# Kernel optimization log

Hardware: AMD Instinct MI355X
Metric: run time of the kernel (lower is better)

## Reference

```python
import jax, jax.numpy as jnp
import numpy as np

B, S, I, H = 2, 400, 80, 128
F = 2 * H            # bidirectional feature dim
N = S + 1            # zero row prepended -> pairwise grid size
MAX_SEG = 50
NCLS = 50


def prelu(x, a):
    return jnp.where(x >= 0, x, a * x)


def lstm_dir(x, Wi, Wh, b, reverse=False):
    # x: (B, S, I); torch gate order: i, f, g, o
    if reverse:
        x = x[:, ::-1]
    Hd = Wh.shape[1]

    def step(carry, xt):
        h, c = carry
        gates = xt @ Wi.T + h @ Wh.T + b
        i_, f_, g_, o_ = jnp.split(gates, 4, axis=-1)
        c = jax.nn.sigmoid(f_) * c + jax.nn.sigmoid(i_) * jnp.tanh(g_)
        h = jax.nn.sigmoid(o_) * jnp.tanh(c)
        return (h, c), h

    h0 = jnp.zeros((x.shape[0], Hd), x.dtype)
    _, hs = jax.lax.scan(step, (h0, h0), jnp.swapaxes(x, 0, 1))
    hs = jnp.swapaxes(hs, 0, 1)
    if reverse:
        hs = hs[:, ::-1]
    return hs


def setup_inputs() -> dict:
    key = jax.random.key(0)
    ks = jax.random.split(key, 16)

    def rn(k, shape, s=0.05):
        return jax.random.normal(k, shape, jnp.float32) * s

    inp = {
        "x": jax.random.normal(ks[0], (B, S, I), jnp.float32),
        "lengths": jnp.full((B,), S, jnp.int32),
        "Wi_f": rn(ks[1], (4 * H, I)), "Wh_f": rn(ks[2], (4 * H, H)), "b_f": jnp.zeros((4 * H,), jnp.float32),
        "Wi_b": rn(ks[3], (4 * H, I)), "Wh_b": rn(ks[4], (4 * H, H)), "b_b": jnp.zeros((4 * H,), jnp.float32),
        "a1": jnp.full((1,), 0.25, jnp.float32),
        "W1": rn(ks[5], (100, 3 * F)), "b1": jnp.zeros((100,), jnp.float32),
        "a2": jnp.full((1,), 0.25, jnp.float32),
        "W2": rn(ks[6], (1, 100)), "b2": jnp.zeros((1,), jnp.float32),
        "ac1": jnp.full((1,), 0.25, jnp.float32),
        "Wc1": rn(ks[7], (2 * NCLS, F)), "bc1": jnp.zeros((2 * NCLS,), jnp.float32),
        "ac2": jnp.full((1,), 0.25, jnp.float32),
        "Wc2": rn(ks[8], (NCLS, 2 * NCLS)), "bc2": jnp.zeros((NCLS,), jnp.float32),
        "ab1": jnp.full((1,), 0.25, jnp.float32),
        "Wb1": rn(ks[9], (2 * NCLS, F)), "bb1": jnp.zeros((2 * NCLS,), jnp.float32),
        "ab2": jnp.full((1,), 0.25, jnp.float32),
        "Wb2": rn(ks[10], (2, 2 * NCLS)), "bb2": jnp.zeros((2,), jnp.float32),
    }
    return inp


def compute_scores(x, Wi_f, Wh_f, b_f, Wi_b, Wh_b, b_b, a1, W1, b1, a2, W2, b2):
    rnn_out = jnp.concatenate(
        [lstm_dir(x, Wi_f, Wh_f, b_f, False), lstm_dir(x, Wi_b, Wh_b, b_b, True)], axis=-1
    )  # (B, S, F)
    xp = jnp.concatenate([jnp.zeros((x.shape[0], 1, F), x.dtype), rnn_out], axis=1)  # (B, N, F)
    cum = jnp.cumsum(xp, axis=1)
    # phi[b,i,j] = concat(cum[j]-cum[i], xp[i], xp[j]); PReLU is elementwise with a
    # single shared parameter, and the first Linear is additive across the concat
    # blocks, so we decompose W1 instead of materializing the (B,N,N,3F) tensor.
    W1c, W1d, W1e = W1[:, :F], W1[:, F:2 * F], W1[:, 2 * F:]
    pc = prelu(cum[:, None, :, :] - cum[:, :, None, :], a1)  # (B, N, N, F)
    pxd = prelu(xp, a1) @ W1d.T                              # (B, N, 100)
    pxe = prelu(xp, a1) @ W1e.T                              # (B, N, 100)
    h = jnp.einsum('bijf,kf->bijk', pc, W1c) + pxd[:, :, None, :] + pxe[:, None, :, :] + b1
    scores = (prelu(h, a2) @ W2.T + b2)[..., 0]              # (B, N, N)
    return rnn_out, scores


def segment_search(scores):
    # DP: best[i] = max_{max(0,i-MAX_SEG) <= k < i} best[k] + scores[:, k, i]
    Bn, Nn = scores.shape[0], scores.shape[1]
    ks = jnp.arange(Nn)

    def dp_step(best, i):
        col = jnp.take(scores, i, axis=2)                    # (B, N)
        mask = (ks >= i - MAX_SEG) & (ks < i)
        cand = jnp.where(mask[None, :], best + col, -jnp.inf)
        m = cand.max(axis=1)
        k = cand.argmax(axis=1)
        best = best.at[:, i].set(m)
        return best, k

    best0 = jnp.zeros((Bn, Nn), scores.dtype)
    best, prev_tail = jax.lax.scan(dp_step, best0, jnp.arange(1, Nn))
    prev = jnp.concatenate([jnp.zeros((Bn, 1), jnp.int32),
                            prev_tail.T.astype(jnp.int32)], axis=1)  # (B, N)
    return best, prev


def reference(x, lengths, Wi_f, Wh_f, b_f, Wi_b, Wh_b, b_b, a1, W1, b1, a2, W2, b2,
              ac1, Wc1, bc1, ac2, Wc2, bc2, ab1, Wb1, bb1, ab2, Wb2, bb2):
    rnn_out, scores = compute_scores(x, Wi_f, Wh_f, b_f, Wi_b, Wh_b, b_b,
                                     a1, W1, b1, a2, W2, b2)
    cls_out = prelu(prelu(rnn_out, ac1) @ Wc1.T + bc1, ac2) @ Wc2.T + bc2
    bin_out = prelu(prelu(rnn_out, ab1) @ Wb1.T + bb1, ab2) @ Wb2.T + bb2
    best, prev = segment_search(scores)
    # pred score for the best segmentation ending at `lengths[b]` equals best[b, L]
    pred_scores = best[jnp.arange(scores.shape[0]), lengths]
    return scores, cls_out, bin_out, pred_scores, prev
```

## Files before the change

### kernel.cpp

```cpp
#include <hip/hip_runtime.h>
#include <hip/hip_fp16.h>
#include <math.h>

#define BB 2
#define SS 400
#define II 80
#define HH 128
#define FF 256
#define NN 401
#define G4 512
#define MAXSEG 50
#define NCLS 50
#define KH 100
#define KP 112
#define FRAGF 14336

#define SCORES_OFF 0
#define CLS_OFF    (BB*NN*NN)
#define BIN_OFF    (CLS_OFF + BB*SS*NCLS)
#define PRED_OFF   (BIN_OFF + BB*SS*2)
#define PREV_OFF   (PRED_OFF + BB)

#define WS_GX      0
#define WS_RNN     (WS_GX + 4*SS*G4)
#define WS_CUM     (WS_RNN + BB*SS*FF)
#define WS_PXD     (WS_CUM + BB*NN*FF)
#define WS_PXE     (WS_PXD + BB*NN*KP)
#define WS_PART    (WS_PXE + BB*NN*KP)
#define WS_W2P     (WS_PART + BB*16*FF)
#define WS_B1P     (WS_W2P + KP)
#define WS_WHP     (WS_B1P + KP)
#define WS_WFRAGC  (WS_WHP + 65536)
#define WS_WFRAGD  (WS_WFRAGC + FRAGF)
#define WS_WFRAGE  (WS_WFRAGD + FRAGF)
#define WS_WFRAGHC (WS_WFRAGE + FRAGF)
#define WS_WFRAGHB (WS_WFRAGHC + FRAGF)
#define WS_BC1P    (WS_WFRAGHB + FRAGF)
#define WS_BB1P    (WS_BC1P + KP)

typedef __attribute__((ext_vector_type(8))) short short8;
typedef __attribute__((ext_vector_type(4))) float f32x4;
typedef _Float16 f16x2 __attribute__((ext_vector_type(2)));
typedef _Float16 f16x8 __attribute__((ext_vector_type(8)));

__device__ __forceinline__ float prelu_f(float x, float a) {
    return x >= 0.f ? x : a * x;
}
__device__ __forceinline__ unsigned short f2bf(float x) {
    union { float f; unsigned u; } v; v.f = x;
    unsigned r = v.u + 0x7fffu + ((v.u >> 16) & 1u);
    return (unsigned short)(r >> 16);
}
__device__ __forceinline__ float fast_sigmoid(float x) {
    return 1.f / (1.f + __expf(-x));
}
__device__ __forceinline__ float fast_tanh(float x) {
    return 1.f - 2.f / (1.f + __expf(2.f * x));
}
__device__ __forceinline__ void barrier_lds() {
    asm volatile("s_waitcnt lgkmcnt(0)\ns_barrier" ::: "memory");
}
__device__ __forceinline__ void rec_barrier() {
    __builtin_amdgcn_sched_barrier(0);
    asm volatile("s_waitcnt lgkmcnt(0)");
    __builtin_amdgcn_s_barrier();
    __builtin_amdgcn_sched_barrier(0);
}
__device__ __forceinline__ int fragidx(int k, int f) {
    int kt = k >> 4, l15 = k & 15;
    int ks = f >> 5, quad = (f >> 3) & 3, e = f & 7;
    return ((((kt * 8 + ks) * 4 + quad) * 16) + l15) * 8 + e;
}

#define WPACKS (5 * KP)
#define PREPBLKS (WPACKS + G4)
__global__ void k_lstm_pre(const float* __restrict__ x,
                           const float* __restrict__ Wi_f, const float* __restrict__ b_f,
                           const float* __restrict__ Wi_b, const float* __restrict__ b_b,
                           float* __restrict__ gx,
                           const float* __restrict__ W1, const float* __restrict__ W2,
                           const float* __restrict__ b1,
                           const float* __restrict__ Wh_f, const float* __restrict__ Wh_b,
                           const float* __restrict__ Wc1, const float* __restrict__ Wb1,
                           const float* __restrict__ bc1, const float* __restrict__ bb1,
                           short* __restrict__ wfC, short* __restrict__ wfD,
                           short* __restrict__ wfE, short* __restrict__ wfHC,
                           short* __restrict__ wfHB,
                           float* __restrict__ w2p, float* __restrict__ b1p,
                           float* __restrict__ bc1p, float* __restrict__ bb1p,
                           __half* __restrict__ whp) {
    int blk0 = blockIdx.x;
    int tid = threadIdx.x;
    if (blk0 < WPACKS) {
        int which = blk0 / KP;
        int k = blk0 % KP;
        float w = 0.f;
        short* dst = wfC;
        if (which == 0)      { if (k < KH) w = W1[k * (3 * FF) + tid];          dst = wfC; }
        else if (which == 1) { if (k < KH) w = W1[k * (3 * FF) + FF + tid];     dst = wfD; }
        else if (which == 2) { if (k < KH) w = W1[k * (3 * FF) + 2 * FF + tid]; dst = wfE; }
        else if (which == 3) { if (k < KH) w = Wc1[k * FF + tid];               dst = wfHC; }
        else                 { if (k < KH) w = Wb1[k * FF + tid];               dst = wfHB; }
        dst[fragidx(k, tid)] = (short)f2bf(w);
        if (tid == 0) {
            if (which == 0) {
                w2p[k] = (k < KH) ? W2[k] : 0.f;
                b1p[k] = (k < KH) ? b1[k] : 0.f;
            } else if (which == 3) {
                bc1p[k] = (k < KH) ? bc1[k] : 0.f;
            } else if (which == 4) {
                bb1p[k] = (k < KH) ? bb1[k] : 0.f;
            }
        }
        return;
    }
    if (blk0 < PREPBLKS) {
        int gq = blk0 - WPACKS;
        int gate = gq >> 7;
        int unit = gq & 127;
        int wv = unit >> 4, col = unit & 15;
        int dir = tid >> 7, k = tid & 127;
        int kt = k >> 5, lanehi = (k >> 3) & 3, e = k & 7;
        int lane = lanehi * 16 + col;
        const float* Wh = dir ? Wh_b : Wh_f;
        whp[(size_t)(((((dir * 4 + gate) * 8 + wv) * 4 + kt) * 64) + lane) * 8 + e] =
            (__half)Wh[gq * HH + k];
        return;
    }
    int blk = blk0 - PREPBLKS;
    int t = blk % SS;
    int db = blk / SS;
    int b = db & 1, dir = db >> 1;
    const float* Wi = dir ? Wi_b : Wi_f;
    const float* bias = dir ? b_b : b_f;
    int xt = dir ? (SS - 1 - t) : t;

    __shared__ __align__(16) float xr[II];
    if (tid < II) xr[tid] = x[(b * SS + xt) * II + tid];
    __syncthreads();

    for (int g = tid; g < G4; g += 256) {
        const float* w = Wi + g * II;
        float acc = bias[g];
#pragma unroll
        for (int i = 0; i < II; i += 4) {
            float4 w4 = *(const float4*)(w + i);
            acc += w4.x * xr[i] + w4.y * xr[i + 1] + w4.z * xr[i + 2] + w4.w * xr[i + 3];
        }
        gx[((size_t)(db * SS + t) * HH + (g & 127)) * 4 + (g >> 7)] = acc;
    }
}

__global__ __launch_bounds__(256, 1)
void k_lstm_rec(const _Float16* __restrict__ whf, const float* __restrict__ gxr,
                float* __restrict__ rnn_out) {
    int db = blockIdx.x;
    int b = db & 1, dir = db >> 1;
    int tid = threadIdx.x;
    int wv = tid >> 6;
    int lane = tid & 63;

    f16x8 bfA[4][4], bfB[4][4];
    {
        const f16x8* wp = (const f16x8*)whf;
#pragma unroll
        for (int g = 0; g < 4; ++g)
#pragma unroll
            for (int kt = 0; kt < 4; ++kt) {
                bfA[g][kt] = wp[((((dir * 4 + g) * 8 + (2 * wv)) * 4 + kt) * 64) + lane];
                bfB[g][kt] = wp[((((dir * 4 + g) * 8 + (2 * wv + 1)) * 4 + kt) * 64) + lane];
            }
    }

    __shared__ __align__(16) __half hsf[2][128];
    (&hsf[0][0])[tid] = (__half)0.f;
    __syncthreads();

    bool act = (lane < 32);
    bool grpB = (lane >= 16);
    int unit = (wv << 5) + (lane & 31);
    float c_state = 0.f;

    const float4* gp4 = (const float4*)gxr + (size_t)(db * SS) * HH + unit;
    float4 g0 = make_float4(0,0,0,0), g1 = g0, g2 = g0, g3 = g0;
    if (act) {
        g0 = gp4[0 * HH];
        g1 = gp4[1 * HH];
        g2 = gp4[2 * HH];
        g3 = gp4[3 * HH];
    }
    const float4* gq = gp4 + (size_t)4 * HH;

    float* outp = rnn_out + ((size_t)b * SS + (dir ? (SS - 1) : 0)) * FF
                + dir * HH + unit;
    const int ostep = dir ? -FF : FF;

    const f32x4 z4 = (f32x4){0.f, 0.f, 0.f, 0.f};
    int pb = 0;
    int hib = (lane >> 4) * 8;
    bool aload = (lane & 3) == 0;

    f16x8 a0v = (f16x8)(_Float16)0.f, a1v = a0v, a2v = a0v, a3v = a0v;

#define REC_STEP(G, PF) do {                                                   \
        if (aload) {                                                           \
            a0v = *(const f16x8*)(&hsf[pb][ 0 + hib]);                         \
            a1v = *(const f16x8*)(&hsf[pb][32 + hib]);                         \
            a2v = *(const f16x8*)(&hsf[pb][64 + hib]);                         \
            a3v = *(const f16x8*)(&hsf[pb][96 + hib]);                         \
        }                                                                      \
        f32x4 aA0 = __builtin_amdgcn_mfma_f32_16x16x32_f16(a0v, bfA[0][0], z4, 0, 0, 0); \
        f32x4 aA1 = __builtin_amdgcn_mfma_f32_16x16x32_f16(a0v, bfA[1][0], z4, 0, 0, 0); \
        f32x4 aA2 = __builtin_amdgcn_mfma_f32_16x16x32_f16(a0v, bfA[2][0], z4, 0, 0, 0); \
        f32x4 aA3 = __builtin_amdgcn_mfma_f32_16x16x32_f16(a0v, bfA[3][0], z4, 0, 0, 0); \
        f32x4 aB0 = __builtin_amdgcn_mfma_f32_16x16x32_f16(a0v, bfB[0][0], z4, 0, 0, 0); \
        f32x4 aB1 = __builtin_amdgcn_mfma_f32_16x16x32_f16(a0v, bfB[1][0], z4, 0, 0, 0); \
        f32x4 aB2 = __builtin_amdgcn_mfma_f32_16x16x32_f16(a0v, bfB[2][0], z4, 0, 0, 0); \
        f32x4 aB3 = __builtin_amdgcn_mfma_f32_16x16x32_f16(a0v, bfB[3][0], z4, 0, 0, 0); \
        aA0 = __builtin_amdgcn_mfma_f32_16x16x32_f16(a1v, bfA[0][1], aA0, 0, 0, 0); \
        aA1 = __builtin_amdgcn_mfma_f32_16x16x32_f16(a1v, bfA[1][1], aA1, 0, 0, 0); \
        aA2 = __builtin_amdgcn_mfma_f32_16x16x32_f16(a1v, bfA[2][1], aA2, 0, 0, 0); \
        aA3 = __builtin_amdgcn_mfma_f32_16x16x32_f16(a1v, bfA[3][1], aA3, 0, 0, 0); \
        aB0 = __builtin_amdgcn_mfma_f32_16x16x32_f16(a1v, bfB[0][1], aB0, 0, 0, 0); \
        aB1 = __builtin_amdgcn_mfma_f32_16x16x32_f16(a1v, bfB[1][1], aB1, 0, 0, 0); \
        aB2 = __builtin_amdgcn_mfma_f32_16x16x32_f16(a1v, bfB[2][1], aB2, 0, 0, 0); \
        aB3 = __builtin_amdgcn_mfma_f32_16x16x32_f16(a1v, bfB[3][1], aB3, 0, 0, 0); \
        aA0 = __builtin_amdgcn_mfma_f32_16x16x32_f16(a2v, bfA[0][2], aA0, 0, 0, 0); \
        aA1 = __builtin_amdgcn_mfma_f32_16x16x32_f16(a2v, bfA[1][2], aA1, 0, 0, 0); \
        aA2 = __builtin_amdgcn_mfma_f32_16x16x32_f16(a2v, bfA[2][2], aA2, 0, 0, 0); \
        aA3 = __builtin_amdgcn_mfma_f32_16x16x32_f16(a2v, bfA[3][2], aA3, 0, 0, 0); \
        aB0 = __builtin_amdgcn_mfma_f32_16x16x32_f16(a2v, bfB[0][2], aB0, 0, 0, 0); \
        aB1 = __builtin_amdgcn_mfma_f32_16x16x32_f16(a2v, bfB[1][2], aB1, 0, 0, 0); \
        aB2 = __builtin_amdgcn_mfma_f32_16x16x32_f16(a2v, bfB[2][2], aB2, 0, 0, 0); \
        aB3 = __builtin_amdgcn_mfma_f32_16x16x32_f16(a2v, bfB[3][2], aB3, 0, 0, 0); \
        aA0 = __builtin_amdgcn_mfma_f32_16x16x32_f16(a3v, bfA[0][3], aA0, 0, 0, 0); \
        aA1 = __builtin_amdgcn_mfma_f32_16x16x32_f16(a3v, bfA[1][3], aA1, 0, 0, 0); \
        aA2 = __builtin_amdgcn_mfma_f32_16x16x32_f16(a3v, bfA[2][3], aA2, 0, 0, 0); \
        aA3 = __builtin_amdgcn_mfma_f32_16x16x32_f16(a3v, bfA[3][3], aA3, 0, 0, 0); \
        aB0 = __builtin_amdgcn_mfma_f32_16x16x32_f16(a3v, bfB[0][3], aB0, 0, 0, 0); \
        aB1 = __builtin_amdgcn_mfma_f32_16x16x32_f16(a3v, bfB[1][3], aB1, 0, 0, 0); \
        aB2 = __builtin_amdgcn_mfma_f32_16x16x32_f16(a3v, bfB[2][3], aB2, 0, 0, 0); \
        aB3 = __builtin_amdgcn_mfma_f32_16x16x32_f16(a3v, bfB[3][3], aB3, 0, 0, 0); \
        if (act) {                                                             \
            float gi = (grpB ? aB0[0] : aA0[0]) + G.x;                         \
            float gf = (grpB ? aB1[0] : aA1[0]) + G.y;                         \
            float gg = (grpB ? aB2[0] : aA2[0]) + G.z;                         \
            float go = (grpB ? aB3[0] : aA3[0]) + G.w;                         \
            if (PF) { G = *gq; gq += HH; }         \
            c_state = fast_sigmoid(gf) * c_state + fast_sigmoid(gi) * fast_tanh(gg); \
            float h = fast_sigmoid(go) * fast_tanh(c_state);                   \
            hsf[pb ^ 1][unit] = (__half)h;                                     \
            *outp = h;                                                         \
            outp += ostep;                                                     \
        }                                                                      \
        rec_barrier();                                                         \
        pb ^= 1;                                                               \
    } while (0)

    for (int it = 0; it < 99; ++it) {
        REC_STEP(g0, 1);
        REC_STEP(g1, 1);
        REC_STEP(g2, 1);
        REC_STEP(g3, 1);
    }
    REC_STEP(g0, 0);
    REC_STEP(g1, 0);
    REC_STEP(g2, 0);
    REC_STEP(g3, 0);
#undef REC_STEP
}

#define PXBLKS 26
#define HDBLKS 25
#define AP 272
#define UCP 116
__global__ __launch_bounds__(256, 2)
void k_cum_mlp(const float* __restrict__ rnn, float* __restrict__ cum,
               const float* __restrict__ a1p,
               const float* __restrict__ ac1p, const float* __restrict__ ab1p,
               const short* __restrict__ wfD, const short* __restrict__ wfE,
               const short* __restrict__ wfHC, const short* __restrict__ wfHB,
               const float* __restrict__ bc1p, const float* __restrict__ bb1p,
               const float* __restrict__ ac2p, const float* __restrict__ ab2p,
               const float* __restrict__ Wc2, const float* __restrict__ bc2,
               const float* __restrict__ Wb2, const float* __restrict__ bb2,
               float* __restrict__ pxd, float* __restrict__ pxe,
               float* __restrict__ cls_out, float* __restrict__ bin_out) {
    int tid = threadIdx.x;
    if (blockIdx.x < BB) {
        int b = blockIdx.x;
        int f = tid;
        float run = 0.f;
        cum[(size_t)(b * NN) * FF + f] = 0.f;
        const float* rp = rnn + (size_t)b * SS * FF + f;
        float* cp = cum + ((size_t)b * NN + 1) * FF + f;
#pragma unroll 8
        for (int t = 0; t < SS; ++t) {
            run += rp[(size_t)t * FF];
            cp[(size_t)t * FF] = run;
        }
        return;
    }
    int blk = blockIdx.x - BB;
    bool is_px = (blk < PXBLKS);
    int rowbase = is_px ? blk * 32 : (blk - PXBLKS) * 32;
    int nrows_tot = is_px ? BB * NN : BB * SS;

    __shared__ __align__(16) short dth[2][32][AP];
    __shared__ float ucsh[2][32][UCP];

    {
        int row = tid >> 3;
        int fb = (tid & 7) * 32;
        int rg = rowbase + row;
        float src[32];
        if (is_px) {
            float a1 = a1p[0];
            int b = rg / NN, n = rg % NN;
            bool valid = (rg < nrows_tot) && (n > 0);
            const float* sp = valid ? (rnn + (b * SS + n - 1) * FF + fb) : nullptr;
#pragma unroll
            for (int c4 = 0; c4 < 8; ++c4) {
                float4 v = valid ? *(const float4*)(sp + c4 * 4) : make_float4(0,0,0,0);
                src[c4*4] = v.x; src[c4*4+1] = v.y; src[c4*4+2] = v.z; src[c4*4+3] = v.w;
            }
            union { short8 s; unsigned short u[8]; } h8;
#pragma unroll
            for (int c8 = 0; c8 < 4; ++c8) {
#pragma unroll
                for (int e = 0; e < 8; ++e) h8.u[e] = f2bf(prelu_f(src[c8*8+e], a1));
                *(short8*)(&dth[0][row][fb + c8 * 8]) = h8.s;
            }
        } else {
            float ac1 = ac1p[0], ab1 = ab1p[0];
            bool valid = (rg < nrows_tot);
            const float* sp = valid ? (rnn + rg * FF + fb) : nullptr;
#pragma unroll
            for (int c4 = 0; c4 < 8; ++c4) {
                float4 v = valid ? *(const float4*)(sp + c4 * 4) : make_float4(0,0,0,0);
                src[c4*4] = v.x; src[c4*4+1] = v.y; src[c4*4+2] = v.z; src[c4*4+3] = v.w;
            }
            union { short8 s; unsigned short u[8]; } hc, hb;
#pragma unroll
            for (int c8 = 0; c8 < 4; ++c8) {
#pragma unroll
                for (int e = 0; e < 8; ++e) {
                    hc.u[e] = f2bf(prelu_f(src[c8*8+e], ac1));
                    hb.u[e] = f2bf(prelu_f(src[c8*8+e], ab1));
                }
                *(short8*)(&dth[0][row][fb + c8 * 8]) = hc.s;
                *(short8*)(&dth[1][row][fb + c8 * 8]) = hb.s;
            }
        }
    }
    __syncthreads();

    int lane = tid & 63;
    int wv = tid >> 6;
    int quad = lane >> 4;
    int l15 = lane & 15;
    int kt0 = wv * 2, kt1 = wv * 2 + 1;
    bool has1 = (kt1 < 7);

    const short8* wp0 = (const short8*)(is_px ? wfD : wfHC);
    const short8* wp1 = (const short8*)(is_px ? wfE : wfHB);

    f32x4 acc[2][2][2];
#pragma unroll
    for (int p = 0; p < 2; ++p)
#pragma unroll
        for (int mt = 0; mt < 2; ++mt)
#pragma unroll
            for (int kk = 0; kk < 2; ++kk) acc[p][mt][kk] = (f32x4){0.f,0.f,0.f,0.f};

#pragma unroll
    for (int ks = 0; ks < 8; ++ks) {
        short8 b00 = wp0[((kt0 * 8 + ks) * 4 + quad) * 16 + l15];
        short8 b01 = has1 ? wp0[((kt1 * 8 + ks) * 4 + quad) * 16 + l15] : b00;
        short8 b10 = wp1[((kt0 * 8 + ks) * 4 + quad) * 16 + l15];
        short8 b11 = has1 ? wp1[((kt1 * 8 + ks) * 4 + quad) * 16 + l15] : b10;
#pragma unroll
        for (int mt = 0; mt < 2; ++mt) {
            short8 a0 = *(const short8*)(&dth[0][mt * 16 + l15][ks * 32 + quad * 8]);
            short8 a1v = is_px ? a0
                       : *(const short8*)(&dth[1][mt * 16 + l15][ks * 32 + quad * 8]);
            acc[0][mt][0] = __builtin_amdgcn_mfma_f32_16x16x32_bf16(a0, b00, acc[0][mt][0], 0, 0, 0);
            acc[1][mt][0] = __builtin_amdgcn_mfma_f32_16x16x32_bf16(a1v, b10, acc[1][mt][0], 0, 0, 0);
            if (has1) {
                acc[0][mt][1] = __builtin_amdgcn_mfma_f32_16x16x32_bf16(a0, b01, acc[0][mt][1], 0, 0, 0);
                acc[1][mt][1] = __builtin_amdgcn_mfma_f32_16x16x32_bf16(a1v, b11, acc[1][mt][1], 0, 0, 0);
            }
        }
    }

    int kout0 = kt0 * 16 + l15;
    int kout1 = has1 ? (kt1 * 16 + l15) : 0;

    if (is_px) {
#pragma unroll
        for (int mt = 0; mt < 2; ++mt) {
#pragma unroll
            for (int r = 0; r < 4; ++r) {
                int m = mt * 16 + quad * 4 + r;
                int rg = rowbase + m;
                if (rg < nrows_tot) {
                    pxd[rg * KP + kout0] = acc[0][mt][0][r];
                    pxe[rg * KP + kout0] = acc[1][mt][0][r];
                    if (has1) {
                        pxd[rg * KP + kout1] = acc[0][mt][1][r];
                        pxe[rg * KP + kout1] = acc[1][mt][1][r];
                    }
                }
            }
        }
        return;
    }

    float bc0 = bc1p[kout0], bc1v = bc1p[kout1];
    float bb0 = bb1p[kout0], bb1v = bb1p[kout1];
    float ac2 = ac2p[0], ab2 = ab2p[0];
#pragma unroll
    for (int mt = 0; mt < 2; ++mt) {
#pragma unroll
        for (int r = 0; r < 4; ++r) {
            int m = mt * 16 + quad * 4 + r;
            ucsh[0][m][kout0] = prelu_f(acc[0][mt][0][r] + bc0, ac2);
            ucsh[1][m][kout0] = prelu_f(acc[1][mt][0][r] + bb0, ab2);
            if (has1) {
                ucsh[0][m][kout1] = prelu_f(acc[0][mt][1][r] + bc1v, ac2);
                ucsh[1][m][kout1] = prelu_f(acc[1][mt][1][r] + bb1v, ab2);
            }
        }
    }
    __syncthreads();
    {
        int row = tid >> 3;
        int oc = tid & 7;
        int rg = rowbase + row;
        bool valid = (rg < nrows_tot);
        for (int o = oc; o < NCLS; o += 8) {
            float s = bc2[o];
            const float* w = Wc2 + o * KH;
#pragma unroll 4
            for (int k = 0; k < KH; ++k) s += w[k] * ucsh[0][row][k];
            if (valid) cls_out[rg * NCLS + o] = s;
        }
        if (tid < 64) {
            int row2 = tid >> 1, o = tid & 1;
            int rg2 = rowbase + row2;
            float s = bb2[o];
            const float* w = Wb2 + o * KH;
#pragma unroll 4
            for (int k = 0; k < KH; ++k) s += w[k] * ucsh[1][row2][k];
            if (rg2 < nrows_tot) bin_out[rg2 * 2 + o] = s;
        }
    }
}

#define JT 32
#define JTILES 13
#define NP2 201
#define APS 280
#define CIP 264
__global__ __launch_bounds__(256, 3)
void k_scores(const float* __restrict__ cum,
              const short* __restrict__ wfrag,
              const float* __restrict__ pxd, const float* __restrict__ pxe,
              const float* __restrict__ b1p, const float* __restrict__ w2p,
              const float* __restrict__ b2p,
              const float* __restrict__ a1p, const float* __restrict__ a2p,
              float* __restrict__ scores, float* __restrict__ dpcol) {
    int blk = blockIdx.x;
    int jt = blk % JTILES;
    int ipair = (blk / JTILES) % NP2;
    int b = blk / (JTILES * NP2);
    int tid = threadIdx.x;
    float a1 = a1p[0], a2 = a2p[0];
    int jbase = jt * JT;
    int i0 = ipair * 2;
    int i1 = i0 + 1;
    bool has_i1 = (i1 <= SS);
    int i1c = has_i1 ? i1 : i0;

    __shared__ __align__(16) float cish[2][CIP];
    __shared__ __align__(16) short dth[2][JT][APS];
    __shared__ float red[2][4][JT];

    cish[0][tid + (tid >> 5)] = cum[(b * NN + i0) * FF + tid];
    cish[1][tid + (tid >> 5)] = cum[(b * NN + i1c) * FF + tid];
    __syncthreads();

    {
        int row = tid >> 3;
        int fb = (tid & 7) * 32;
        int fbq = fb + (tid & 7);
        int jg = jbase + row;
        int jc = (jg <= SS) ? jg : SS;
        const float* cj = cum + (b * NN + jc) * FF + fb;
        float4 v[8];
#pragma unroll
        for (int c8 = 0; c8 < 4; ++c8) {
            v[2 * c8] = *(const float4*)(cj + c8 * 8);
            v[2 * c8 + 1] = *(const float4*)(cj + c8 * 8 + 4);
        }
#pragma unroll
        for (int ii = 0; ii < 2; ++ii) {
            const float* cio = &cish[ii][0];
#pragma unroll
            for (int c8 = 0; c8 < 4; ++c8) {
                float dv[8] = { v[2*c8].x, v[2*c8].y, v[2*c8].z, v[2*c8].w,
                                v[2*c8+1].x, v[2*c8+1].y, v[2*c8+1].z, v[2*c8+1].w };
                union { short8 s; unsigned short u[8]; } h8;
#pragma unroll
                for (int e = 0; e < 8; ++e) {
                    float d = prelu_f(dv[e] - cio[fbq + c8 * 8 + e], a1);
                    h8.u[e] = f2bf(d);
                }
                *(short8*)(&dth[ii][row][fb + c8 * 8]) = h8.s;
            }
        }
    }
    __syncthreads();

    int lane = tid & 63;
    int wv = tid >> 6;
    int quad = lane >> 4;
    int l15 = lane & 15;
    int kt0 = wv * 2, kt1 = wv * 2 + 1;
    bool has1 = (kt1 < 7);

    const short8* wf = (const short8*)wfrag;
    f32x4 acc[2][2][2];
#pragma unroll
    for (int ii = 0; ii < 2; ++ii)
#pragma unroll
        for (int mt = 0; mt < 2; ++mt)
#pragma unroll
            for (int kk = 0; kk < 2; ++kk) acc[ii][mt][kk] = (f32x4){0.f,0.f,0.f,0.f};

#pragma unroll
    for (int ks = 0; ks < 8; ++ks) {
        short8 b0 = wf[((kt0 * 8 + ks) * 4 + quad) * 16 + l15];
        short8 b1v = has1 ? wf[((kt1 * 8 + ks) * 4 + quad) * 16 + l15] : b0;
#pragma unroll
        for (int ii = 0; ii < 2; ++ii) {
#pragma unroll
            for (int mt = 0; mt < 2; ++mt) {
                short8 a = *(const short8*)(&dth[ii][mt * 16 + l15][ks * 32 + quad * 8]);
                acc[ii][mt][0] = __builtin_amdgcn_mfma_f32_16x16x32_bf16(a, b0, acc[ii][mt][0], 0, 0, 0);
                if (has1)
                    acc[ii][mt][1] = __builtin_amdgcn_mfma_f32_16x16x32_bf16(a, b1v, acc[ii][mt][1], 0, 0, 0);
            }
        }
    }

    int kout0 = kt0 * 16 + l15;
    int kout1 = has1 ? (kt1 * 16 + l15) : 0;
    float bb0 = b1p[kout0], bb1v = b1p[kout1];
    float w20 = w2p[kout0];
    float w21 = has1 ? w2p[kout1] : 0.f;

#pragma unroll
    for (int ii = 0; ii < 2; ++ii) {
        int iv = ii ? i1c : i0;
        float pd0 = pxd[(b * NN + iv) * KP + kout0];
        float pd1 = pxd[(b * NN + iv) * KP + kout1];
#pragma unroll
        for (int mt = 0; mt < 2; ++mt) {
#pragma unroll
            for (int r = 0; r < 4; ++r) {
                int m = mt * 16 + quad * 4 + r;
                int jg = jbase + m;
                int jc = (jg <= SS) ? jg : SS;
                float pe0 = pxe[(b * NN + jc) * KP + kout0];
                float pe1 = pxe[(b * NN + jc) * KP + kout1];
                float h0 = acc[ii][mt][0][r] + pd0 + pe0 + bb0;
                float s = w20 * prelu_f(h0, a2);
                float h1 = acc[ii][mt][1][r] + pd1 + pe1 + bb1v;
                s += w21 * prelu_f(h1, a2);
                s += __shfl_xor(s, 1);
                s += __shfl_xor(s, 2);
                s += __shfl_xor(s, 4);
                s += __shfl_xor(s, 8);
                if (l15 == 0) red[ii][wv][m] = s;
            }
        }
    }
    __syncthreads();
    if (tid < 2 * JT) {
        int ii = tid >> 5;
        int jl = tid & 31;
        int jg = jbase + jl;
        int iv = ii ? i1 : i0;
        if (jg <= SS && (ii == 0 || has_i1)) {
            float tot = red[ii][0][jl] + red[ii][1][jl] + red[ii][2][jl] + red[ii][3][jl] + b2p[0];
            scores[(b * NN + iv) * NN + jg] = tot;
            int d = jg - iv;
            if (d >= 1 && d <= MAXSEG) {
                dpcol[(b * NN + jg) * 64 + (iv & 63)] = tot;
            }
        }
    }
}

__global__ void k_dp(const float* __restrict__ dpcol, const int* __restrict__ lengths,
                     float* __restrict__ predF, float* __restrict__ prevF) {
    int b = blockIdx.x;
    int lane = threadIdx.x;
    int len = lengths[b];
    if (lane == 0) prevF[b * NN] = 0.f;

    float blr = 0.f;
    float predv = 0.f;

#define LO(I) (((I) > MAXSEG) ? ((I) - MAXSEG) : 0)
#define LOADCOL(ii) \
    ( ((ii) <= SS && (((lane - LO(ii)) & 63) < ((ii) - LO(ii)))) \
        ? dpcol[(b * NN + (ii)) * 64 + lane] : 0.f )

    float u0 = LOADCOL(1), u1 = LOADCOL(2), u2 = LOADCOL(3), u3 = LOADCOL(4);
    float u4 = LOADCOL(5), u5 = LOADCOL(6), u6 = LOADCOL(7), u7 = LOADCOL(8);

#define DPP_MAX(CTRL, v) do {                                                 \
        int _t = __builtin_amdgcn_update_dpp(__float_as_int(v),               \
                     __float_as_int(v), (CTRL), 0xF, 0xF, false);             \
        (v) = fmaxf((v), __int_as_float(_t));                                 \
    } while (0)

#define DP_STEP(I, BUF) do {                                                  \
        int lo_ = LO(I);                                                      \
        int cnt_ = (I) - lo_;                                                 \
        int off_ = (lane - lo_) & 63;                                         \
        float v0_ = (off_ < cnt_) ? blr + BUF : -INFINITY;                    \
        float v_ = v0_;                                                       \
        DPP_MAX(0x111, v_);                                   \
        DPP_MAX(0x112, v_);                                   \
        DPP_MAX(0x114, v_);                                   \
        DPP_MAX(0x118, v_);                                   \
        DPP_MAX(0x142, v_);                                 \
        DPP_MAX(0x143, v_);                                 \
        float m_ = __int_as_float(                                            \
            __builtin_amdgcn_readlane(__float_as_int(v_), 63));               \
        unsigned long long mk_ = __ballot(v0_ == m_);                         \
        int rot_ = lo_ & 63;                                                  \
        unsigned long long mr_ = rot_ ? ((mk_ >> rot_) | (mk_ << (64 - rot_))) \
                                      : mk_;                                  \
        int kb_ = lo_ + (__ffsll(mr_) - 1);                                   \
        if (lane == 0) {                                                      \
            prevF[b * NN + (I)] = (float)kb_;                                 \
            if ((I) == len) predv = m_;                                       \
        }                                                                     \
        if (lane == ((I) & 63)) blr = m_;                                     \
    } while (0)

    for (int i = 1; i <= SS; i += 8) {
        DP_STEP(i, u0);     u0 = LOADCOL(i + 8);
        DP_STEP(i + 1, u1); u1 = LOADCOL(i + 9);
        DP_STEP(i + 2, u2); u2 = LOADCOL(i + 10);
        DP_STEP(i + 3, u3); u3 = LOADCOL(i + 11);
        DP_STEP(i + 4, u4); u4 = LOADCOL(i + 12);
        DP_STEP(i + 5, u5); u5 = LOADCOL(i + 13);
        DP_STEP(i + 6, u6); u6 = LOADCOL(i + 14);
        DP_STEP(i + 7, u7); u7 = LOADCOL(i + 15);
    }
#undef DP_STEP
#undef DPP_MAX
#undef LOADCOL
#undef LO
    if (lane == 0) predF[b] = predv;
}

extern "C" void kernel_launch(void* const* d_in, const int* in_sizes, int n_in,
                              void* d_out, int out_size, void* d_ws, size_t ws_size,
                              hipStream_t stream) {
    const float* x    = (const float*)d_in[0];
    const int* lengths= (const int*)d_in[1];
    const float* Wi_f = (const float*)d_in[2];
    const float* Wh_f = (const float*)d_in[3];
    const float* b_f  = (const float*)d_in[4];
    const float* Wi_b = (const float*)d_in[5];
    const float* Wh_b = (const float*)d_in[6];
    const float* b_b  = (const float*)d_in[7];
    const float* a1   = (const float*)d_in[8];
    const float* W1   = (const float*)d_in[9];
    const float* b1   = (const float*)d_in[10];
    const float* a2   = (const float*)d_in[11];
    const float* W2   = (const float*)d_in[12];
    const float* b2   = (const float*)d_in[13];
    const float* ac1  = (const float*)d_in[14];
    const float* Wc1  = (const float*)d_in[15];
    const float* bc1  = (const float*)d_in[16];
    const float* ac2  = (const float*)d_in[17];
    const float* Wc2  = (const float*)d_in[18];
    const float* bc2  = (const float*)d_in[19];
    const float* ab1  = (const float*)d_in[20];
    const float* Wb1  = (const float*)d_in[21];
    const float* bb1  = (const float*)d_in[22];
    const float* ab2  = (const float*)d_in[23];
    const float* Wb2  = (const float*)d_in[24];
    const float* bb2  = (const float*)d_in[25];

    float* out = (float*)d_out;
    float* scores = out + SCORES_OFF;
    float* cls    = out + CLS_OFF;
    float* bin    = out + BIN_OFF;
    float* pred   = out + PRED_OFF;
    float* prev   = out + PREV_OFF;

    float* ws    = (float*)d_ws;
    float* gx    = ws + WS_GX;
    float* dpcol = ws + WS_GX;
    float* rnn   = ws + WS_RNN;
    float* cum   = ws + WS_CUM;
    float* pxd   = ws + WS_PXD;
    float* pxe   = ws + WS_PXE;
    float* w2p   = ws + WS_W2P;
    float* b1p   = ws + WS_B1P;
    __half* whp  = (__half*)(ws + WS_WHP);
    short* wfC   = (short*)(ws + WS_WFRAGC);
    short* wfD   = (short*)(ws + WS_WFRAGD);
    short* wfE   = (short*)(ws + WS_WFRAGE);
    short* wfHC  = (short*)(ws + WS_WFRAGHC);
    short* wfHB  = (short*)(ws + WS_WFRAGHB);
    float* bc1p  = ws + WS_BC1P;
    float* bb1p  = ws + WS_BB1P;

    k_lstm_pre<<<PREPBLKS + 4 * SS, 256, 0, stream>>>(x, Wi_f, b_f, Wi_b, b_b, gx,
                                                      W1, W2, b1, Wh_f, Wh_b,
                                                      Wc1, Wb1, bc1, bb1,
                                                      wfC, wfD, wfE, wfHC, wfHB,
                                                      w2p, b1p, bc1p, bb1p, whp);
    k_lstm_rec<<<4, 256, 0, stream>>>((const _Float16*)whp, gx, rnn);
    k_cum_mlp<<<BB + PXBLKS + HDBLKS, 256, 0, stream>>>(rnn, cum, a1, ac1, ab1,
                                                        wfD, wfE, wfHC, wfHB,
                                                        bc1p, bb1p, ac2, ab2,
                                                        Wc2, bc2, Wb2, bb2,
                                                        pxd, pxe, cls, bin);
    k_scores<<<BB * NP2 * JTILES, 256, 0, stream>>>(cum, wfC, pxd, pxe, b1p, w2p, b2,
                                                    a1, a2, scores, dpcol);
    k_dp<<<BB, 64, 0, stream>>>(dpcol, lengths, pred, prev);
}
```

Measured before the change: 553.9 us.

## Tile input projection over timesteps, move weight packing into rec kernel, pair DP steps

The input-gate projection now processes 8 timesteps per block, so each thread loads its two weight rows once and reuses them across all 8 steps instead of once per timestep. The MLP weight-fragment packing moves out of the pre kernel and into extra blocks of the recurrent LSTM kernel, where they run alongside the 4 recurrence blocks on otherwise idle CUs. The serial segment DP handles two positions per step: it interleaves two DPP max reductions and fixes up the second position's dependency on the first by reading the score for that edge directly. The paired step adds register pressure and a tie-breaking subtlety in the argmax.

```diff
diff --git a/kernel.cpp b/kernel.cpp
--- a/kernel.cpp
+++ b/kernel.cpp
@@ -57,9 +57,6 @@
 __device__ __forceinline__ float fast_tanh(float x) {
     return 1.f - 2.f / (1.f + __expf(2.f * x));
 }
-__device__ __forceinline__ void barrier_lds() {
-    asm volatile("s_waitcnt lgkmcnt(0)\ns_barrier" ::: "memory");
-}
 __device__ __forceinline__ void rec_barrier() {
     __builtin_amdgcn_sched_barrier(0);
     asm volatile("s_waitcnt lgkmcnt(0)");
@@ -72,26 +69,103 @@
     return ((((kt * 8 + ks) * 4 + quad) * 16) + l15) * 8 + e;
 }
 
-#define WPACKS (5 * KP)
-#define PREPBLKS (WPACKS + G4)
+#define GXTC 8
+#define GXBLKS (4 * (SS / GXTC))
+#define PREPBLKS (G4 + GXBLKS)
 __global__ void k_lstm_pre(const float* __restrict__ x,
                            const float* __restrict__ Wi_f, const float* __restrict__ b_f,
                            const float* __restrict__ Wi_b, const float* __restrict__ b_b,
                            float* __restrict__ gx,
-                           const float* __restrict__ W1, const float* __restrict__ W2,
-                           const float* __restrict__ b1,
                            const float* __restrict__ Wh_f, const float* __restrict__ Wh_b,
-                           const float* __restrict__ Wc1, const float* __restrict__ Wb1,
-                           const float* __restrict__ bc1, const float* __restrict__ bb1,
-                           short* __restrict__ wfC, short* __restrict__ wfD,
-                           short* __restrict__ wfE, short* __restrict__ wfHC,
-                           short* __restrict__ wfHB,
-                           float* __restrict__ w2p, float* __restrict__ b1p,
-                           float* __restrict__ bc1p, float* __restrict__ bb1p,
                            __half* __restrict__ whp) {
     int blk0 = blockIdx.x;
     int tid = threadIdx.x;
-    if (blk0 < WPACKS) {
+    if (blk0 < G4) {
+        int gq = blk0;
+        int gate = gq >> 7;
+        int unit = gq & 127;
+        int wv = unit >> 4, col = unit & 15;
+        int dir = tid >> 7, k = tid & 127;
+        int kt = k >> 5, lanehi = (k >> 3) & 3, e = k & 7;
+        int lane = lanehi * 16 + col;
+        const float* Wh = dir ? Wh_b : Wh_f;
+        whp[(size_t)(((((dir * 4 + gate) * 8 + wv) * 4 + kt) * 64) + lane) * 8 + e] =
+            (__half)Wh[gq * HH + k];
+        return;
+    }
+    int gxb = blk0 - G4;
+    int db = gxb / (SS / GXTC);
+    int tc = gxb % (SS / GXTC);
+    int b = db & 1, dir = db >> 1;
+    const float* Wi = dir ? Wi_b : Wi_f;
+    const float* bias = dir ? b_b : b_f;
+    int t0 = tc * GXTC;
+
+    __shared__ __align__(16) float xs[GXTC][II];
+    for (int idx = tid; idx < GXTC * II; idx += 256) {
+        int tt = idx / II, ii = idx - tt * II;
+        int xt = dir ? (SS - 1 - (t0 + tt)) : (t0 + tt);
+        xs[tt][ii] = x[(b * SS + xt) * II + ii];
+    }
+    __syncthreads();
+
+    int g1 = tid + 256;
+    const float* w0p = Wi + tid * II;
+    const float* w1p = Wi + g1 * II;
+    float acc0[GXTC], acc1[GXTC];
+    {
+        float b0v = bias[tid], b1v = bias[g1];
+#pragma unroll
+        for (int t = 0; t < GXTC; ++t) { acc0[t] = b0v; acc1[t] = b1v; }
+    }
+    for (int kc = 0; kc < 5; ++kc) {
+        float4 wa0 = *(const float4*)(w0p + kc * 16 + 0);
+        float4 wa1 = *(const float4*)(w0p + kc * 16 + 4);
+        float4 wa2 = *(const float4*)(w0p + kc * 16 + 8);
+        float4 wa3 = *(const float4*)(w0p + kc * 16 + 12);
+        float4 wb0 = *(const float4*)(w1p + kc * 16 + 0);
+        float4 wb1 = *(const float4*)(w1p + kc * 16 + 4);
+        float4 wb2 = *(const float4*)(w1p + kc * 16 + 8);
+        float4 wb3 = *(const float4*)(w1p + kc * 16 + 12);
+#pragma unroll
+        for (int t = 0; t < GXTC; ++t) {
+            float4 x0 = *(const float4*)(&xs[t][kc * 16 + 0]);
+            float4 x1 = *(const float4*)(&xs[t][kc * 16 + 4]);
+            float4 x2 = *(const float4*)(&xs[t][kc * 16 + 8]);
+            float4 x3 = *(const float4*)(&xs[t][kc * 16 + 12]);
+            acc0[t] += wa0.x * x0.x + wa0.y * x0.y + wa0.z * x0.z + wa0.w * x0.w;
+            acc0[t] += wa1.x * x1.x + wa1.y * x1.y + wa1.z * x1.z + wa1.w * x1.w;
+            acc0[t] += wa2.x * x2.x + wa2.y * x2.y + wa2.z * x2.z + wa2.w * x2.w;
+            acc0[t] += wa3.x * x3.x + wa3.y * x3.y + wa3.z * x3.z + wa3.w * x3.w;
+            acc1[t] += wb0.x * x0.x + wb0.y * x0.y + wb0.z * x0.z + wb0.w * x0.w;
+            acc1[t] += wb1.x * x1.x + wb1.y * x1.y + wb1.z * x1.z + wb1.w * x1.w;
+            acc1[t] += wb2.x * x2.x + wb2.y * x2.y + wb2.z * x2.z + wb2.w * x2.w;
+            acc1[t] += wb3.x * x3.x + wb3.y * x3.y + wb3.z * x3.z + wb3.w * x3.w;
+        }
+    }
+#pragma unroll
+    for (int t = 0; t < GXTC; ++t) {
+        gx[((size_t)(db * SS + t0 + t) * HH + (tid & 127)) * 4 + (tid >> 7)] = acc0[t];
+        gx[((size_t)(db * SS + t0 + t) * HH + (g1 & 127)) * 4 + (g1 >> 7)] = acc1[t];
+    }
+}
+
+#define WPACKS (5 * KP)
+__global__ __launch_bounds__(256, 1)
+void k_lstm_rec(const _Float16* __restrict__ whf, const float* __restrict__ gxr,
+                float* __restrict__ rnn_out,
+                const float* __restrict__ W1, const float* __restrict__ W2,
+                const float* __restrict__ b1,
+                const float* __restrict__ Wc1, const float* __restrict__ Wb1,
+                const float* __restrict__ bc1, const float* __restrict__ bb1,
+                short* __restrict__ wfC, short* __restrict__ wfD,
+                short* __restrict__ wfE, short* __restrict__ wfHC,
+                short* __restrict__ wfHB,
+                float* __restrict__ w2p, float* __restrict__ b1p,
+                float* __restrict__ bc1p, float* __restrict__ bb1p) {
+    int tid = threadIdx.x;
+    if (blockIdx.x >= 4) {
+        int blk0 = blockIdx.x - 4;
         int which = blk0 / KP;
         int k = blk0 % KP;
         float w = 0.f;
@@ -114,49 +188,8 @@
         }
         return;
     }
-    if (blk0 < PREPBLKS) {
-        int gq = blk0 - WPACKS;
-        int gate = gq >> 7;
-        int unit = gq & 127;
-        int wv = unit >> 4, col = unit & 15;
-        int dir = tid >> 7, k = tid & 127;
-        int kt = k >> 5, lanehi = (k >> 3) & 3, e = k & 7;
-        int lane = lanehi * 16 + col;
-        const float* Wh = dir ? Wh_b : Wh_f;
-        whp[(size_t)(((((dir * 4 + gate) * 8 + wv) * 4 + kt) * 64) + lane) * 8 + e] =
-            (__half)Wh[gq * HH + k];
-        return;
-    }
-    int blk = blk0 - PREPBLKS;
-    int t = blk % SS;
-    int db = blk / SS;
-    int b = db & 1, dir = db >> 1;
-    const float* Wi = dir ? Wi_b : Wi_f;
-    const float* bias = dir ? b_b : b_f;
-    int xt = dir ? (SS - 1 - t) : t;
-
-    __shared__ __align__(16) float xr[II];
-    if (tid < II) xr[tid] = x[(b * SS + xt) * II + tid];
-    __syncthreads();
-
-    for (int g = tid; g < G4; g += 256) {
-        const float* w = Wi + g * II;
-        float acc = bias[g];
-#pragma unroll
-        for (int i = 0; i < II; i += 4) {
-            float4 w4 = *(const float4*)(w + i);
-            acc += w4.x * xr[i] + w4.y * xr[i + 1] + w4.z * xr[i + 2] + w4.w * xr[i + 3];
-        }
-        gx[((size_t)(db * SS + t) * HH + (g & 127)) * 4 + (g >> 7)] = acc;
-    }
-}
-
-__global__ __launch_bounds__(256, 1)
-void k_lstm_rec(const _Float16* __restrict__ whf, const float* __restrict__ gxr,
-                float* __restrict__ rnn_out) {
     int db = blockIdx.x;
     int b = db & 1, dir = db >> 1;
-    int tid = threadIdx.x;
     int wv = tid >> 6;
     int lane = tid & 63;
 
@@ -621,50 +654,66 @@
     float u0 = LOADCOL(1), u1 = LOADCOL(2), u2 = LOADCOL(3), u3 = LOADCOL(4);
     float u4 = LOADCOL(5), u5 = LOADCOL(6), u6 = LOADCOL(7), u7 = LOADCOL(8);
 
-#define DPP_MAX(CTRL, v) do {                                                 \
-        int _t = __builtin_amdgcn_update_dpp(__float_as_int(v),               \
-                     __float_as_int(v), (CTRL), 0xF, 0xF, false);             \
-        (v) = fmaxf((v), __int_as_float(_t));                                 \
+#define DPP_MAX2(CTRL, va, vb) do {                                           \
+        int _ta = __builtin_amdgcn_update_dpp(__float_as_int(va),             \
+                      __float_as_int(va), (CTRL), 0xF, 0xF, false);           \
+        int _tb = __builtin_amdgcn_update_dpp(__float_as_int(vb),             \
+                      __float_as_int(vb), (CTRL), 0xF, 0xF, false);           \
+        (va) = fmaxf((va), __int_as_float(_ta));                              \
+        (vb) = fmaxf((vb), __int_as_float(_tb));                              \
     } while (0)
 
-#define DP_STEP(I, BUF) do {                                                  \
-        int lo_ = LO(I);                                                      \
-        int cnt_ = (I) - lo_;                                                 \
-        int off_ = (lane - lo_) & 63;                                         \
-        float v0_ = (off_ < cnt_) ? blr + BUF : -INFINITY;                    \
-        float v_ = v0_;                                                       \
-        DPP_MAX(0x111, v_);                                   \
-        DPP_MAX(0x112, v_);                                   \
-        DPP_MAX(0x114, v_);                                   \
-        DPP_MAX(0x118, v_);                                   \
-        DPP_MAX(0x142, v_);                                 \
-        DPP_MAX(0x143, v_);                                 \
-        float m_ = __int_as_float(                                            \
-            __builtin_amdgcn_readlane(__float_as_int(v_), 63));               \
-        unsigned long long mk_ = __ballot(v0_ == m_);                         \
-        int rot_ = lo_ & 63;                                                  \
-        unsigned long long mr_ = rot_ ? ((mk_ >> rot_) | (mk_ << (64 - rot_))) \
-                                      : mk_;                                  \
-        int kb_ = lo_ + (__ffsll(mr_) - 1);                                   \
+#define DP_STEP2(I, BUFA, BUFB) do {                                          \
+        int loA_ = LO(I);                                                     \
+        int cntA_ = (I) - loA_;                                               \
+        int loB_ = LO((I) + 1);                                               \
+        int cntBm_ = (I) - loB_;                   \
+        int offA_ = (lane - loA_) & 63;                                       \
+        int offB_ = (lane - loB_) & 63;                                       \
+        float vA0_ = (offA_ < cntA_) ? blr + BUFA : -INFINITY;                \
+        float vB0_ = (offB_ < cntBm_) ? blr + BUFB : -INFINITY;               \
+        float vA_ = vA0_, vB_ = vB0_;                                         \
+        DPP_MAX2(0x111, vA_, vB_);                            \
+        DPP_MAX2(0x112, vA_, vB_);                            \
+        DPP_MAX2(0x114, vA_, vB_);                            \
+        DPP_MAX2(0x118, vA_, vB_);                            \
+        DPP_MAX2(0x142, vA_, vB_);                          \
+        DPP_MAX2(0x143, vA_, vB_);                          \
+        float mA_ = __int_as_float(                                           \
+            __builtin_amdgcn_readlane(__float_as_int(vA_), 63));              \
+        float mB_ = __int_as_float(                                           \
+            __builtin_amdgcn_readlane(__float_as_int(vB_), 63));              \
+        float sI_ = __int_as_float(                                           \
+            __builtin_amdgcn_readlane(__float_as_int(BUFB), (I) & 63));       \
+        float candI_ = mA_ + sI_;                                             \
+        bool takeI_ = candI_ > mB_;                                           \
+        float mBf_ = takeI_ ? candI_ : mB_;                                   \
+        unsigned long long mkA_ = __ballot(vA0_ == mA_);                      \
+        unsigned long long mkB_ = __ballot(vB0_ == mB_);                      \
+        int rotA_ = loA_ & 63;                                                \
+        int rotB_ = loB_ & 63;                                                \
+        unsigned long long mrA_ = rotA_ ? ((mkA_ >> rotA_) | (mkA_ << (64 - rotA_))) : mkA_; \
+        unsigned long long mrB_ = rotB_ ? ((mkB_ >> rotB_) | (mkB_ << (64 - rotB_))) : mkB_; \
+        int kbA_ = loA_ + (__ffsll(mrA_) - 1);                                \
+        int kbB_ = takeI_ ? (I) : (loB_ + (__ffsll(mrB_) - 1));               \
         if (lane == 0) {                                                      \
-            prevF[b * NN + (I)] = (float)kb_;                                 \
-            if ((I) == len) predv = m_;                                       \
+            prevF[b * NN + (I)] = (float)kbA_;                                \
+            prevF[b * NN + (I) + 1] = (float)kbB_;                            \
+            if ((I) == len) predv = mA_;                                      \
+            if ((I) + 1 == len) predv = mBf_;                                 \
         }                                                                     \
-        if (lane == ((I) & 63)) blr = m_;                                     \
+        if (lane == ((I) & 63)) blr = mA_;                                    \
+        if (lane == (((I) + 1) & 63)) blr = mBf_;                             \
     } while (0)
 
     for (int i = 1; i <= SS; i += 8) {
-        DP_STEP(i, u0);     u0 = LOADCOL(i + 8);
-        DP_STEP(i + 1, u1); u1 = LOADCOL(i + 9);
-        DP_STEP(i + 2, u2); u2 = LOADCOL(i + 10);
-        DP_STEP(i + 3, u3); u3 = LOADCOL(i + 11);
-        DP_STEP(i + 4, u4); u4 = LOADCOL(i + 12);
-        DP_STEP(i + 5, u5); u5 = LOADCOL(i + 13);
-        DP_STEP(i + 6, u6); u6 = LOADCOL(i + 14);
-        DP_STEP(i + 7, u7); u7 = LOADCOL(i + 15);
-    }
-#undef DP_STEP
-#undef DPP_MAX
+        DP_STEP2(i,     u0, u1); u0 = LOADCOL(i + 8);  u1 = LOADCOL(i + 9);
+        DP_STEP2(i + 2, u2, u3); u2 = LOADCOL(i + 10); u3 = LOADCOL(i + 11);
+        DP_STEP2(i + 4, u4, u5); u4 = LOADCOL(i + 12); u5 = LOADCOL(i + 13);
+        DP_STEP2(i + 6, u6, u7); u6 = LOADCOL(i + 14); u7 = LOADCOL(i + 15);
+    }
+#undef DP_STEP2
+#undef DPP_MAX2
 #undef LOADCOL
 #undef LO
     if (lane == 0) predF[b] = predv;
@@ -725,12 +774,12 @@
     float* bc1p  = ws + WS_BC1P;
     float* bb1p  = ws + WS_BB1P;
 
-    k_lstm_pre<<<PREPBLKS + 4 * SS, 256, 0, stream>>>(x, Wi_f, b_f, Wi_b, b_b, gx,
-                                                      W1, W2, b1, Wh_f, Wh_b,
-                                                      Wc1, Wb1, bc1, bb1,
-                                                      wfC, wfD, wfE, wfHC, wfHB,
-                                                      w2p, b1p, bc1p, bb1p, whp);
-    k_lstm_rec<<<4, 256, 0, stream>>>((const _Float16*)whp, gx, rnn);
+    k_lstm_pre<<<PREPBLKS, 256, 0, stream>>>(x, Wi_f, b_f, Wi_b, b_b, gx,
+                                             Wh_f, Wh_b, whp);
+    k_lstm_rec<<<4 + WPACKS, 256, 0, stream>>>((const _Float16*)whp, gx, rnn,
+                                               W1, W2, b1, Wc1, Wb1, bc1, bb1,
+                                               wfC, wfD, wfE, wfHC, wfHB,
+                                               w2p, b1p, bc1p, bb1p);
     k_cum_mlp<<<BB + PXBLKS + HDBLKS, 256, 0, stream>>>(rnn, cum, a1, ac1, ab1,
                                                         wfD, wfE, wfHC, wfHB,
                                                         bc1p, bb1p, ac2, ab2,
```

New measurement: 527.9 us. 1.05x faster.
